# Kernel tuning notes

Measured on AMD Instinct MI355X. Metric: run time of the kernel, lower is better.

## Reference

```python
import jax, jax.numpy as jnp
import numpy as np

D_MODEL = 1024
N_TILES = 16
BATCH = 32768
THRESH = 0.3


def setup_inputs() -> dict:
    key = jax.random.key(0)
    k_x, k_sig, k_w, k_b = jax.random.split(key, 4)
    x = jax.random.normal(k_x, (BATCH, D_MODEL), dtype=jnp.float32)
    # nn.Parameter(torch.randn(n_tiles, d_model) * 0.5)
    signatures_raw = jax.random.normal(k_sig, (N_TILES, D_MODEL), dtype=jnp.float32) * 0.5
    # nn.Linear(d_model, d_model) default init: U(-1/sqrt(fan_in), 1/sqrt(fan_in))
    bound = 1.0 / np.sqrt(D_MODEL)
    W = jax.random.uniform(k_w, (N_TILES, D_MODEL, D_MODEL), dtype=jnp.float32, minval=-bound, maxval=bound)
    b = jax.random.uniform(k_b, (N_TILES, D_MODEL), dtype=jnp.float32, minval=-bound, maxval=bound)
    return {"x": x, "signatures_raw": signatures_raw, "W": W, "b": b}


def _quantize_ternary(s):
    # straight-through ternary: forward value is q, gradient is identity
    q = jnp.where(s > THRESH, 1.0, jnp.where(s < -THRESH, -1.0, 0.0))
    return s + jax.lax.stop_gradient(q - s)


def reference(x, signatures_raw, W, b):
    sigs = _quantize_ternary(signatures_raw)          # [E, D]
    scores = x @ sigs.T                               # [B, E]
    tile_indices = jnp.argmax(scores, axis=-1)        # [B]
    out = jnp.zeros_like(x)
    # fixed small loop over experts: masked combine of per-expert Linear+ReLU
    for e in range(N_TILES):
        y = jax.nn.relu(x @ W[e].T + b[e])            # [B, D]
        out = out + jnp.where((tile_indices == e)[:, None], y, 0.0)
    out = out + x                                     # residual
    return out, tile_indices
```

## Files before the change

kernel.cpp:

```cpp
#include <hip/hip_runtime.h>
#include <hip/hip_bf16.h>

#define BATCH   32768
#define DM      1024
#define NE      16
#define THRESHF 0.3f
#define MARGIN  0.02f

#define CTRL_OFF 131072
#define QBF_OFF  139264
#define PERM_OFF 172032
#define XBF_OFF  311296
#define WB_OFF   67420160ull
#define WS_NEED  (WB_OFF + (size_t)NE * DM * DM * 2)

typedef __attribute__((ext_vector_type(8))) short bf16x8;
typedef __attribute__((ext_vector_type(4))) float f32x4;

static __device__ __forceinline__ unsigned short f2bf(float f) {
    union { float f; unsigned u; } v; v.f = f;
    unsigned r = (v.u + 0x7FFFu + ((v.u >> 16) & 1u)) >> 16;
    return (unsigned short)r;
}
static __device__ __forceinline__ float bf2f(unsigned short h) {
    union { unsigned u; float f; } v; v.u = ((unsigned)h) << 16;
    return v.f;
}

static __device__ __forceinline__ void gload_lds16(const void* g, void* s) {
    __builtin_amdgcn_global_load_lds(
        (const __attribute__((address_space(1))) void*)g,
        (__attribute__((address_space(3))) void*)s, 16, 0, 0);
}

__global__ void k_init(const float* __restrict__ sig, unsigned* __restrict__ ctrl,
                       int* __restrict__ perm, unsigned short* __restrict__ Qbf) {
    const int t = blockIdx.x * 256 + threadIdx.x;
    if (t < 544) ctrl[t] = 0;
    if (t < 1024) {
        unsigned pm = 0, mm = 0;
#pragma unroll
        for (int e = 0; e < NE; ++e) {
            float s = sig[e * DM + t];
            pm |= (s > THRESHF ? 1u : 0u) << e;
            mm |= (s < -THRESHF ? 1u : 0u) << e;
        }
        ctrl[1024 + t] = pm | (mm << 16);
    }
    if (t < 8704) ((int4*)perm)[t] = make_int4(0, 0, 0, 0);
    {
        float s = sig[t];
        Qbf[t] = s > THRESHF ? (unsigned short)0x3F80u
                             : (s < -THRESHF ? (unsigned short)0xBF80u : (unsigned short)0u);
    }
}

__global__ __launch_bounds__(256) void k_router(const float* __restrict__ x,
                                                const unsigned short* __restrict__ Qbf,
                                                unsigned* __restrict__ ctrl,
                                                int* __restrict__ idx,
                                                float* __restrict__ outIdx,
                                                unsigned short* __restrict__ Xbf,
                                                int writeXbf) {
    const int t = threadIdx.x, w = t >> 6, l = t & 63;
    const int lc = l & 15, lr = l >> 4;
    const int wid = blockIdx.x * 4 + w;
    const int row0 = wid * 16;
    const unsigned* packT = ctrl + 1024;

    const float* ax = x + (size_t)(row0 + lc) * DM + lr * 8;
    const unsigned short* qx = Qbf + (size_t)lc * DM + lr * 8;
    unsigned short* xb = Xbf + (size_t)(row0 + lc) * DM + lr * 8;

    f32x4 acc = (f32x4){0.f, 0.f, 0.f, 0.f};

    for (int kt = 0; kt < 16; ++kt) {
#pragma unroll
        for (int h = 0; h < 2; ++h) {
            const int ko = kt * 64 + h * 32;
            float4 v0 = *(const float4*)(ax + ko);
            float4 v1 = *(const float4*)(ax + ko + 4);
            bf16x8 q = *(const bf16x8*)(qx + ko);

            float f[8] = {v0.x, v0.y, v0.z, v0.w, v1.x, v1.y, v1.z, v1.w};
            bf16x8 ah, al;
#pragma unroll
            for (int j = 0; j < 8; ++j) {
                unsigned short hi = f2bf(f[j]);
                float r = f[j] - bf2f(hi);
                ah[j] = (short)hi;
                al[j] = (short)f2bf(r);
            }
            if (writeXbf) *(bf16x8*)(xb + ko) = ah;
            acc = __builtin_amdgcn_mfma_f32_16x16x32_bf16(ah, q, acc, 0, 0, 0);
            acc = __builtin_amdgcn_mfma_f32_16x16x32_bf16(al, q, acc, 0, 0, 0);
        }
    }

    float bv[4]; int bi[4]; float gap[4];
#pragma unroll
    for (int reg = 0; reg < 4; ++reg) {
        float v = acc[reg]; int i = lc; float s = -3.4e38f;
#pragma unroll
        for (int m = 1; m < 16; m <<= 1) {
            float ov = __shfl_xor(v, m, 64);
            int oi = __shfl_xor(i, m, 64);
            float os = __shfl_xor(s, m, 64);
            bool take = (ov > v) || (ov == v && oi < i);
            float loser = take ? v : ov;
            v = take ? ov : v;
            i = take ? oi : i;
            s = fmaxf(fmaxf(s, os), loser);
        }
        bv[reg] = v; bi[reg] = i; gap[reg] = v - s;
    }

    unsigned flagsw = 0;
#pragma unroll
    for (int reg = 0; reg < 4; ++reg)
        flagsw |= (gap[reg] < MARGIN ? 1u : 0u) << reg;

    if (__any(lc == 0 && flagsw != 0)) {
#pragma unroll
        for (int reg = 0; reg < 4; ++reg) {
            for (int g = 0; g < 4; ++g) {
                const unsigned fw = __shfl(flagsw, g * 16, 64);
                if ((fw >> reg) & 1u) {
                    const int row = row0 + g * 4 + reg;
                    const float* xr = x + (size_t)row * DM;
                    float xv[16]; unsigned mk[16];
#pragma unroll
                    for (int k2 = 0; k2 < 16; ++k2) {
                        xv[k2] = xr[k2 * 64 + l];
                        mk[k2] = packT[k2 * 64 + l];
                    }
                    double best = 0.0; int bbi = 0;
                    for (int e = 0; e < 16; ++e) {
                        double a = 0.0;
#pragma unroll
                        for (int k2 = 0; k2 < 16; ++k2) {
                            const int pb = (int)((mk[k2] >> e) & 1u);
                            const int mb = (int)((mk[k2] >> (16 + e)) & 1u);
                            a += pb ? (double)xv[k2] : (mb ? -(double)xv[k2] : 0.0);
                        }
#pragma unroll
                        for (int m = 1; m < 64; m <<= 1) a += __shfl_xor(a, m, 64);
                        if (e == 0 || a > best) { best = a; bbi = e; }
                    }
                    if (lr == g && lc == 0) bi[reg] = bbi;
                }
            }
        }
    }

    if (lc == 0) {
#pragma unroll
        for (int reg = 0; reg < 4; ++reg) {
            const int row = row0 + lr * 4 + reg;
            idx[row] = bi[reg];
            outIdx[row] = (float)bi[reg];
            atomicAdd(&ctrl[bi[reg] * 16], 1u);
        }
    }
}

__global__ void k_scan(unsigned* __restrict__ ctrl) {
    if (threadIdx.x == 0) {
        int* tileBase = (int*)(ctrl + 512);
        int acc = 0;
        for (int e = 0; e < NE; ++e) {
            tileBase[e] = acc;
            acc += (int)((ctrl[e * 16] + 127u) / 128u);
        }
        tileBase[NE] = acc;
    }
}

__global__ __launch_bounds__(256) void k_perm(const int* __restrict__ idx,
                                              unsigned* __restrict__ ctrl,
                                              int* __restrict__ perm) {
    __shared__ unsigned hcnt[16];
    __shared__ unsigned hbase[16];
    const int t = threadIdx.x;
    const int row = blockIdx.x * 256 + t;
    const int* tileBase = (const int*)(ctrl + 512);
    if (t < 16) hcnt[t] = 0;
    __syncthreads();
    const int e = idx[row];
    const unsigned lrank = atomicAdd(&hcnt[e], 1u);
    __syncthreads();
    if (t < 16) hbase[t] = atomicAdd(&ctrl[256 + t * 16], hcnt[t]);
    __syncthreads();
    perm[tileBase[e] * 128 + hbase[e] + lrank] = row;
}

__global__ __launch_bounds__(256) void k_convw(const float* __restrict__ W,
                                               unsigned short* __restrict__ Wb) {
    const size_t g = ((size_t)blockIdx.x * 256 + threadIdx.x) * 8;
    float4 a = *(const float4*)&W[g];
    float4 b = *(const float4*)&W[g + 4];
    *(ushort4*)&Wb[g]     = make_ushort4(f2bf(a.x), f2bf(a.y), f2bf(a.z), f2bf(a.w));
    *(ushort4*)&Wb[g + 4] = make_ushort4(f2bf(b.x), f2bf(b.y), f2bf(b.z), f2bf(b.w));
}

template <int MODE>
__global__ __launch_bounds__(256) void k_gemm(const unsigned short* __restrict__ Xbf,
                                              const unsigned short* __restrict__ Wb,
                                              const float* __restrict__ x,
                                              const float* __restrict__ W,
                                              const float* __restrict__ bias,
                                              const int* __restrict__ perm,
                                              const unsigned* __restrict__ ctrl,
                                              float* __restrict__ out) {
    __shared__ unsigned short A_lds[3][128 * 32];
    __shared__ unsigned short B_lds[3][128 * 32];

    const int* tileBase = (const int*)(ctrl + 512);

    int bx, ny;
    {
        const int flat = blockIdx.x;
        const int xcd = flat & 7, s2 = flat >> 3;
        bx = xcd * 34 + (s2 >> 3);
        ny = s2 & 7;
    }
    const int total = tileBase[NE];
    if (bx >= total) return;
    int e = 0;
    while (e < NE - 1 && tileBase[e + 1] <= bx) ++e;
    const int ltile = bx - tileBase[e];
    const int valid = (int)ctrl[e * 16] - ltile * 128;
    const int n0 = ny * 128;

    const int t = threadIdx.x, w = t >> 6, l = t & 63;
    const int wr = w >> 1, wc = w & 1;
    const int lc = l & 15, lr = l >> 4;
    const int hsw = ((t & 3) - ((t >> 3) & 3)) & 3;
    const int ssw = (lr + (lc >> 1)) & 3;

    f32x4 acc[4][4];
#pragma unroll
    for (int m = 0; m < 4; ++m)
#pragma unroll
        for (int n = 0; n < 4; ++n) acc[m][n] = (f32x4){0.f, 0.f, 0.f, 0.f};

    const size_t aRowBase = (size_t)bx * 128;
    const unsigned short* Bg = Wb + ((size_t)e * DM + n0) * DM;

    if (MODE == 0) {
        const int r0 = t >> 2;
        const int prow0 = perm[aRowBase + r0];
        const int prow1 = perm[aRowBase + 64 + r0];
        const unsigned short* a0 = Xbf + (size_t)prow0 * DM + hsw * 8;
        const unsigned short* a1 = Xbf + (size_t)prow1 * DM + hsw * 8;
        const unsigned short* b0 = Bg + (size_t)(t >> 2) * DM + hsw * 8;
        const unsigned short* b1 = Bg + (size_t)(64 + (t >> 2)) * DM + hsw * 8;

        auto STAGE = [&](int kt, int buf) {
            const int ko = kt * 32;
            gload_lds16(a0 + ko, &A_lds[buf][(size_t)(w * 64) * 8]);
            gload_lds16(a1 + ko, &A_lds[buf][(size_t)(256 + w * 64) * 8]);
            gload_lds16(b0 + ko, &B_lds[buf][(size_t)(w * 64) * 8]);
            gload_lds16(b1 + ko, &B_lds[buf][(size_t)(256 + w * 64) * 8]);
        };

        STAGE(0, 0);
        STAGE(1, 1);

        const int NT = DM / 32;
        int cur = 0;
        for (int kt = 0; kt < NT; ++kt) {
            if (kt + 1 < NT) asm volatile("s_waitcnt vmcnt(4)" ::: "memory");
            else             asm volatile("s_waitcnt vmcnt(0)" ::: "memory");
            __builtin_amdgcn_sched_barrier(0);
            __builtin_amdgcn_s_barrier();
            __builtin_amdgcn_sched_barrier(0);

            if (kt + 2 < NT) {
                const int nb = (cur + 2 >= 3) ? cur - 1 : cur + 2;
                STAGE(kt + 2, nb);
            }

            bf16x8 af[4], bf[4];
#pragma unroll
            for (int m = 0; m < 4; ++m)
                af[m] = *(const bf16x8*)&A_lds[cur][(wr * 64 + m * 16 + lc) * 32 + ssw * 8];
#pragma unroll
            for (int n = 0; n < 4; ++n)
                bf[n] = *(const bf16x8*)&B_lds[cur][(wc * 64 + n * 16 + lc) * 32 + ssw * 8];
#pragma unroll
            for (int m = 0; m < 4; ++m)
#pragma unroll
                for (int n = 0; n < 4; ++n)
                    acc[m][n] = __builtin_amdgcn_mfma_f32_16x16x32_bf16(af[m], bf[n], acc[m][n], 0, 0, 0);

            cur = (cur + 1 >= 3) ? 0 : cur + 1;
        }
    } else {
        for (int kt = 0; kt < DM / 32; ++kt) {
            __syncthreads();
#pragma unroll
            for (int rd = 0; rd < 2; ++rd) {
                const int c = rd * 256 + t;
                const int r = c >> 2;
                const float* wp = W + ((size_t)e * DM + n0 + r) * DM + kt * 32 + hsw * 8;
                float4 q0 = *(const float4*)wp;
                float4 q1 = *(const float4*)(wp + 4);
                *(ushort4*)&B_lds[0][c * 8]     = make_ushort4(f2bf(q0.x), f2bf(q0.y), f2bf(q0.z), f2bf(q0.w));
                *(ushort4*)&B_lds[0][c * 8 + 4] = make_ushort4(f2bf(q1.x), f2bf(q1.y), f2bf(q1.z), f2bf(q1.w));
                ushort4 p0 = make_ushort4(0, 0, 0, 0), p1 = p0;
                if (r < valid) {
                    const int orow = perm[aRowBase + r];
                    const float* xp = x + (size_t)orow * DM + kt * 32 + hsw * 8;
                    float4 u0 = *(const float4*)xp;
                    float4 u1 = *(const float4*)(xp + 4);
                    p0 = make_ushort4(f2bf(u0.x), f2bf(u0.y), f2bf(u0.z), f2bf(u0.w));
                    p1 = make_ushort4(f2bf(u1.x), f2bf(u1.y), f2bf(u1.z), f2bf(u1.w));
                }
                *(ushort4*)&A_lds[0][c * 8]     = p0;
                *(ushort4*)&A_lds[0][c * 8 + 4] = p1;
            }
            __syncthreads();

            bf16x8 af[4], bf[4];
#pragma unroll
            for (int m = 0; m < 4; ++m)
                af[m] = *(const bf16x8*)&A_lds[0][(wr * 64 + m * 16 + lc) * 32 + ssw * 8];
#pragma unroll
            for (int n = 0; n < 4; ++n)
                bf[n] = *(const bf16x8*)&B_lds[0][(wc * 64 + n * 16 + lc) * 32 + ssw * 8];
#pragma unroll
            for (int m = 0; m < 4; ++m)
#pragma unroll
                for (int n = 0; n < 4; ++n)
                    acc[m][n] = __builtin_amdgcn_mfma_f32_16x16x32_bf16(af[m], bf[n], acc[m][n], 0, 0, 0);
        }
    }

    float bvv[4];
#pragma unroll
    for (int n = 0; n < 4; ++n) bvv[n] = bias[e * DM + n0 + wc * 64 + n * 16 + lc];

#pragma unroll
    for (int m = 0; m < 4; ++m) {
#pragma unroll
        for (int reg = 0; reg < 4; ++reg) {
            const int rit = wr * 64 + m * 16 + lr * 4 + reg;
            if (rit < valid) {
                const int orow = perm[aRowBase + rit];
                float* op = out + (size_t)orow * DM;
                if (MODE == 0) {
                    const unsigned short* xr = Xbf + (size_t)orow * DM;
#pragma unroll
                    for (int n = 0; n < 4; ++n) {
                        const int col = n0 + wc * 64 + n * 16 + lc;
                        float v = acc[m][n][reg] + bvv[n];
                        v = v > 0.f ? v : 0.f;
                        op[col] = v + bf2f(xr[col]);
                    }
                } else {
                    const float* xr = x + (size_t)orow * DM;
#pragma unroll
                    for (int n = 0; n < 4; ++n) {
                        const int col = n0 + wc * 64 + n * 16 + lc;
                        float v = acc[m][n][reg] + bvv[n];
                        v = v > 0.f ? v : 0.f;
                        op[col] = v + xr[col];
                    }
                }
            }
        }
    }
}

extern "C" void kernel_launch(void* const* d_in, const int* in_sizes, int n_in,
                              void* d_out, int out_size, void* d_ws, size_t ws_size,
                              hipStream_t stream) {
    const float* x    = (const float*)d_in[0];
    const float* sig  = (const float*)d_in[1];
    const float* W    = (const float*)d_in[2];
    const float* bias = (const float*)d_in[3];
    float* out = (float*)d_out;
    float* outIdx = out + (size_t)BATCH * DM;

    char* ws = (char*)d_ws;
    int* idx = (int*)ws;
    unsigned* ctrl = (unsigned*)(ws + CTRL_OFF);
    unsigned short* Qbf = (unsigned short*)(ws + QBF_OFF);
    int* perm = (int*)(ws + PERM_OFF);
    unsigned short* Xbf = (unsigned short*)(ws + XBF_OFF);
    unsigned short* Wb = (unsigned short*)(ws + WB_OFF);

    const bool full = ws_size >= WS_NEED;

    k_init<<<64, 256, 0, stream>>>(sig, ctrl, perm, Qbf);
    k_router<<<512, 256, 0, stream>>>(x, Qbf, ctrl, idx, outIdx, Xbf, full ? 1 : 0);
    k_scan<<<1, 64, 0, stream>>>(ctrl);
    k_perm<<<128, 256, 0, stream>>>(idx, ctrl, perm);
    if (full) {
        k_convw<<<8192, 256, 0, stream>>>(W, Wb);
        k_gemm<0><<<2176, 256, 0, stream>>>(Xbf, Wb, x, W, bias, perm, ctrl, out);
    } else {
        k_gemm<1><<<2176, 256, 0, stream>>>(Xbf, Wb, x, W, bias, perm, ctrl, out);
    }
}
```

Before: 247.8 us.

## Replace 128x128 expert GEMM with 256x256 tile, 512-thread double-buffered kernel

Replaces the grouped expert GEMM with a new kernel using 256x256 output tiles, 8 waves, a double-buffered LDS pipeline with a K-step of 64, swizzled LDS addressing, interleaved async global-to-LDS loads, and setprio around MFMA bursts. Routing groups are padded to 256 rows, so perm and scan take a group size G. The larger tiles are meant to raise arithmetic intensity and cut L2/HBM traffic for A and B. The cost is more padding waste per expert, fewer blocks (576), and higher register and LDS pressure.

```diff
diff --git a/kernel.cpp b/kernel.cpp
--- a/kernel.cpp
+++ b/kernel.cpp
@@ -10,12 +10,14 @@
 #define CTRL_OFF 131072
 #define QBF_OFF  139264
 #define PERM_OFF 172032
-#define XBF_OFF  311296
-#define WB_OFF   67420160ull
+#define XBF_OFF  319488
+#define WB_OFF   67428352ull
 #define WS_NEED  (WB_OFF + (size_t)NE * DM * DM * 2)
 
 typedef __attribute__((ext_vector_type(8))) short bf16x8;
 typedef __attribute__((ext_vector_type(4))) float f32x4;
+
+#define MFMA16(a, b, c) __builtin_amdgcn_mfma_f32_16x16x32_bf16(a, b, c, 0, 0, 0)
 
 static __device__ __forceinline__ unsigned short f2bf(float f) {
     union { float f; unsigned u; } v; v.f = f;
@@ -47,7 +49,7 @@
         }
         ctrl[1024 + t] = pm | (mm << 16);
     }
-    if (t < 8704) ((int4*)perm)[t] = make_int4(0, 0, 0, 0);
+    if (t < 9216) ((int4*)perm)[t] = make_int4(0, 0, 0, 0);
     {
         float s = sig[t];
         Qbf[t] = s > THRESHF ? (unsigned short)0x3F80u
@@ -92,8 +94,8 @@
                 al[j] = (short)f2bf(r);
             }
             if (writeXbf) *(bf16x8*)(xb + ko) = ah;
-            acc = __builtin_amdgcn_mfma_f32_16x16x32_bf16(ah, q, acc, 0, 0, 0);
-            acc = __builtin_amdgcn_mfma_f32_16x16x32_bf16(al, q, acc, 0, 0, 0);
+            acc = MFMA16(ah, q, acc);
+            acc = MFMA16(al, q, acc);
         }
     }
 
@@ -164,13 +166,13 @@
     }
 }
 
-__global__ void k_scan(unsigned* __restrict__ ctrl) {
+__global__ void k_scan(unsigned* __restrict__ ctrl, int G) {
     if (threadIdx.x == 0) {
         int* tileBase = (int*)(ctrl + 512);
         int acc = 0;
         for (int e = 0; e < NE; ++e) {
             tileBase[e] = acc;
-            acc += (int)((ctrl[e * 16] + 127u) / 128u);
+            acc += (int)((ctrl[e * 16] + (unsigned)(G - 1)) / (unsigned)G);
         }
         tileBase[NE] = acc;
     }
@@ -178,7 +180,7 @@
 
 __global__ __launch_bounds__(256) void k_perm(const int* __restrict__ idx,
                                               unsigned* __restrict__ ctrl,
-                                              int* __restrict__ perm) {
+                                              int* __restrict__ perm, int G) {
     __shared__ unsigned hcnt[16];
     __shared__ unsigned hbase[16];
     const int t = threadIdx.x;
@@ -191,7 +193,7 @@
     __syncthreads();
     if (t < 16) hbase[t] = atomicAdd(&ctrl[256 + t * 16], hcnt[t]);
     __syncthreads();
-    perm[tileBase[e] * 128 + hbase[e] + lrank] = row;
+    perm[tileBase[e] * G + hbase[e] + lrank] = row;
 }
 
 __global__ __launch_bounds__(256) void k_convw(const float* __restrict__ W,
@@ -203,20 +205,208 @@
     *(ushort4*)&Wb[g + 4] = make_ushort4(f2bf(b.x), f2bf(b.y), f2bf(b.z), f2bf(b.w));
 }
 
-template <int MODE>
-__global__ __launch_bounds__(256) void k_gemm(const unsigned short* __restrict__ Xbf,
-                                              const unsigned short* __restrict__ Wb,
-                                              const float* __restrict__ x,
-                                              const float* __restrict__ W,
-                                              const float* __restrict__ bias,
-                                              const int* __restrict__ perm,
-                                              const unsigned* __restrict__ ctrl,
-                                              float* __restrict__ out) {
-    __shared__ unsigned short A_lds[3][128 * 32];
-    __shared__ unsigned short B_lds[3][128 * 32];
+#define LDA(Ab, mf, ks) \
+    (*(const bf16x8*)&(Ab)[(((wr * 128 + (mf) * 16 + lc) * 8 + \
+                             (((ks) * 4 + lr + (lc & 7)) & 7)) * 8)])
+#define LDB(Bb, nf, ks) \
+    (*(const bf16x8*)&(Bb)[(((wc * 64 + (nf) * 16 + lc) * 8 + \
+                             (((ks) * 4 + lr + (lc & 7)) & 7)) * 8)])
+
+__global__ __launch_bounds__(512, 2) void k_gemm256(
+        const unsigned short* __restrict__ Xbf,
+        const unsigned short* __restrict__ Wb,
+        const float* __restrict__ bias,
+        const int* __restrict__ perm,
+        const unsigned* __restrict__ ctrl,
+        float* __restrict__ out) {
+    __shared__ unsigned short Al[2][16384];
+    __shared__ unsigned short Bl[2][16384];
 
     const int* tileBase = (const int*)(ctrl + 512);
-
+    int bx, ny;
+    {
+        const int flat = blockIdx.x;
+        const int xcd = flat & 7, s2 = flat >> 3;
+        bx = xcd * 18 + (s2 >> 2);
+        ny = s2 & 3;
+    }
+    const int total = tileBase[NE];
+    if (bx >= total) return;
+    int e = 0;
+    while (e < NE - 1 && tileBase[e + 1] <= bx) ++e;
+    const int valid = (int)ctrl[e * 16] - (bx - tileBase[e]) * 256;
+    const int n0 = ny * 256;
+
+    const int t = threadIdx.x, w = t >> 6, l = t & 63;
+    const int lc = l & 15, lr = l >> 4;
+    const int wr = w >> 2, wc = w & 3;
+    const int j = (w << 3) + (l >> 3);
+    const int d = ((l & 7) - (l >> 3)) & 7;
+    const size_t prB = (size_t)bx * 256;
+
+    const unsigned short* asrc[4];
+    const unsigned short* bsrc[4];
+    int aB[4], bB[4];
+#pragma unroll
+    for (int q = 0; q < 4; ++q) {
+        const int ra = q * 32 + (j & 31) + (j >> 5) * 128;
+        asrc[q] = Xbf + (size_t)perm[prB + ra] * DM + d * 8;
+        const int rb = (j >> 4) * 64 + q * 16 + (j & 15);
+        bsrc[q] = Wb + ((size_t)e * DM + n0 + rb) * DM + d * 8;
+        aB[q] = (q * 256 + (w >> 2) * 1024 + (w & 3) * 64) * 8;
+        bB[q] = ((w >> 1) * 512 + q * 128 + (w & 1) * 64) * 8;
+    }
+
+    f32x4 acc[8][4];
+#pragma unroll
+    for (int m = 0; m < 8; ++m)
+#pragma unroll
+        for (int n = 0; n < 4; ++n) acc[m][n] = (f32x4){0.f, 0.f, 0.f, 0.f};
+
+#pragma unroll
+    for (int q = 0; q < 4; ++q) gload_lds16(bsrc[q], &Bl[0][bB[q]]);
+#pragma unroll
+    for (int q = 0; q < 4; ++q) gload_lds16(asrc[q], &Al[0][aB[q]]);
+
+    const int NT = DM / 64;
+    for (int kt = 0; kt < NT; ++kt) {
+        const int buf = kt & 1;
+        const unsigned short* Ab = Al[buf];
+        const unsigned short* Bb = Bl[buf];
+        unsigned short* An = Al[buf ^ 1];
+        unsigned short* Bn = Bl[buf ^ 1];
+        const int ko = (kt + 1) * 64;
+        const bool more = (kt + 1 < NT);
+
+        if (more) {
+            gload_lds16(bsrc[0] + ko, Bn + bB[0]);
+            gload_lds16(bsrc[1] + ko, Bn + bB[1]);
+            asm volatile("s_waitcnt vmcnt(2)" ::: "memory");
+        } else {
+            asm volatile("s_waitcnt vmcnt(0)" ::: "memory");
+        }
+        __builtin_amdgcn_sched_barrier(0);
+        __builtin_amdgcn_s_barrier();
+        __builtin_amdgcn_sched_barrier(0);
+
+        bf16x8 bfr[4][2];
+#pragma unroll
+        for (int nf = 0; nf < 4; ++nf) {
+            bfr[nf][0] = LDB(Bb, nf, 0);
+            bfr[nf][1] = LDB(Bb, nf, 1);
+        }
+        {
+            bf16x8 a00 = LDA(Ab, 0, 0), a01 = LDA(Ab, 0, 1);
+            bf16x8 a10 = LDA(Ab, 1, 0), a11 = LDA(Ab, 1, 1);
+            __builtin_amdgcn_s_setprio(1);
+#pragma unroll
+            for (int nf = 0; nf < 4; ++nf) {
+                acc[0][nf] = MFMA16(a00, bfr[nf][0], acc[0][nf]);
+                acc[0][nf] = MFMA16(a01, bfr[nf][1], acc[0][nf]);
+                acc[1][nf] = MFMA16(a10, bfr[nf][0], acc[1][nf]);
+                acc[1][nf] = MFMA16(a11, bfr[nf][1], acc[1][nf]);
+            }
+            __builtin_amdgcn_s_setprio(0);
+        }
+        __builtin_amdgcn_s_barrier();
+
+        {
+            bf16x8 a00 = LDA(Ab, 2, 0), a01 = LDA(Ab, 2, 1);
+            bf16x8 a10 = LDA(Ab, 3, 0), a11 = LDA(Ab, 3, 1);
+            if (more) {
+                gload_lds16(bsrc[2] + ko, Bn + bB[2]);
+                gload_lds16(bsrc[3] + ko, Bn + bB[3]);
+            }
+            __builtin_amdgcn_s_barrier();
+            __builtin_amdgcn_sched_barrier(0);
+            __builtin_amdgcn_s_setprio(1);
+#pragma unroll
+            for (int nf = 0; nf < 4; ++nf) {
+                acc[2][nf] = MFMA16(a00, bfr[nf][0], acc[2][nf]);
+                acc[2][nf] = MFMA16(a01, bfr[nf][1], acc[2][nf]);
+                acc[3][nf] = MFMA16(a10, bfr[nf][0], acc[3][nf]);
+                acc[3][nf] = MFMA16(a11, bfr[nf][1], acc[3][nf]);
+            }
+            __builtin_amdgcn_s_setprio(0);
+        }
+        __builtin_amdgcn_s_barrier();
+
+        {
+            bf16x8 a00 = LDA(Ab, 4, 0), a01 = LDA(Ab, 4, 1);
+            bf16x8 a10 = LDA(Ab, 5, 0), a11 = LDA(Ab, 5, 1);
+            if (more) {
+                gload_lds16(asrc[0] + ko, An + aB[0]);
+                gload_lds16(asrc[1] + ko, An + aB[1]);
+            }
+            __builtin_amdgcn_s_barrier();
+            __builtin_amdgcn_sched_barrier(0);
+            __builtin_amdgcn_s_setprio(1);
+#pragma unroll
+            for (int nf = 0; nf < 4; ++nf) {
+                acc[4][nf] = MFMA16(a00, bfr[nf][0], acc[4][nf]);
+                acc[4][nf] = MFMA16(a01, bfr[nf][1], acc[4][nf]);
+                acc[5][nf] = MFMA16(a10, bfr[nf][0], acc[5][nf]);
+                acc[5][nf] = MFMA16(a11, bfr[nf][1], acc[5][nf]);
+            }
+            __builtin_amdgcn_s_setprio(0);
+        }
+        __builtin_amdgcn_s_barrier();
+
+        {
+            bf16x8 a00 = LDA(Ab, 6, 0), a01 = LDA(Ab, 6, 1);
+            bf16x8 a10 = LDA(Ab, 7, 0), a11 = LDA(Ab, 7, 1);
+            if (more) {
+                gload_lds16(asrc[2] + ko, An + aB[2]);
+                gload_lds16(asrc[3] + ko, An + aB[3]);
+            }
+            __builtin_amdgcn_s_barrier();
+            __builtin_amdgcn_sched_barrier(0);
+            __builtin_amdgcn_s_setprio(1);
+#pragma unroll
+            for (int nf = 0; nf < 4; ++nf) {
+                acc[6][nf] = MFMA16(a00, bfr[nf][0], acc[6][nf]);
+                acc[6][nf] = MFMA16(a01, bfr[nf][1], acc[6][nf]);
+                acc[7][nf] = MFMA16(a10, bfr[nf][0], acc[7][nf]);
+                acc[7][nf] = MFMA16(a11, bfr[nf][1], acc[7][nf]);
+            }
+            __builtin_amdgcn_s_setprio(0);
+        }
+        __builtin_amdgcn_s_barrier();
+    }
+
+    float bvv[4];
+#pragma unroll
+    for (int nf = 0; nf < 4; ++nf)
+        bvv[nf] = bias[e * DM + n0 + wc * 64 + nf * 16 + lc];
+
+#pragma unroll
+    for (int mf = 0; mf < 8; ++mf) {
+#pragma unroll
+        for (int reg = 0; reg < 4; ++reg) {
+            const int rit = wr * 128 + mf * 16 + lr * 4 + reg;
+            if (rit < valid) {
+                const int orow = perm[prB + rit];
+                float* op = out + (size_t)orow * DM;
+                const unsigned short* xr = Xbf + (size_t)orow * DM;
+#pragma unroll
+                for (int nf = 0; nf < 4; ++nf) {
+                    const int col = n0 + wc * 64 + nf * 16 + lc;
+                    float v = acc[mf][nf][reg] + bvv[nf];
+                    v = v > 0.f ? v : 0.f;
+                    op[col] = v + bf2f(xr[col]);
+                }
+            }
+        }
+    }
+}
+
+__global__ __launch_bounds__(256) void k_gemm_small(
+        const float* __restrict__ x, const float* __restrict__ W,
+        const float* __restrict__ bias, const int* __restrict__ perm,
+        const unsigned* __restrict__ ctrl, float* __restrict__ out) {
+    __shared__ unsigned short A_lds[128 * 32];
+    __shared__ unsigned short B_lds[128 * 32];
+    const int* tileBase = (const int*)(ctrl + 512);
     int bx, ny;
     {
         const int flat = blockIdx.x;
@@ -228,10 +418,8 @@
     if (bx >= total) return;
     int e = 0;
     while (e < NE - 1 && tileBase[e + 1] <= bx) ++e;
-    const int ltile = bx - tileBase[e];
-    const int valid = (int)ctrl[e * 16] - ltile * 128;
+    const int valid = (int)ctrl[e * 16] - (bx - tileBase[e]) * 128;
     const int n0 = ny * 128;
-
     const int t = threadIdx.x, w = t >> 6, l = t & 63;
     const int wr = w >> 1, wc = w & 1;
     const int lc = l & 15, lr = l >> 4;
@@ -243,134 +431,67 @@
     for (int m = 0; m < 4; ++m)
 #pragma unroll
         for (int n = 0; n < 4; ++n) acc[m][n] = (f32x4){0.f, 0.f, 0.f, 0.f};
-
     const size_t aRowBase = (size_t)bx * 128;
-    const unsigned short* Bg = Wb + ((size_t)e * DM + n0) * DM;
-
-    if (MODE == 0) {
-        const int r0 = t >> 2;
-        const int prow0 = perm[aRowBase + r0];
-        const int prow1 = perm[aRowBase + 64 + r0];
-        const unsigned short* a0 = Xbf + (size_t)prow0 * DM + hsw * 8;
-        const unsigned short* a1 = Xbf + (size_t)prow1 * DM + hsw * 8;
-        const unsigned short* b0 = Bg + (size_t)(t >> 2) * DM + hsw * 8;
-        const unsigned short* b1 = Bg + (size_t)(64 + (t >> 2)) * DM + hsw * 8;
-
-        auto STAGE = [&](int kt, int buf) {
-            const int ko = kt * 32;
-            gload_lds16(a0 + ko, &A_lds[buf][(size_t)(w * 64) * 8]);
-            gload_lds16(a1 + ko, &A_lds[buf][(size_t)(256 + w * 64) * 8]);
-            gload_lds16(b0 + ko, &B_lds[buf][(size_t)(w * 64) * 8]);
-            gload_lds16(b1 + ko, &B_lds[buf][(size_t)(256 + w * 64) * 8]);
-        };
-
-        STAGE(0, 0);
-        STAGE(1, 1);
-
-        const int NT = DM / 32;
-        int cur = 0;
-        for (int kt = 0; kt < NT; ++kt) {
-            if (kt + 1 < NT) asm volatile("s_waitcnt vmcnt(4)" ::: "memory");
-            else             asm volatile("s_waitcnt vmcnt(0)" ::: "memory");
-            __builtin_amdgcn_sched_barrier(0);
-            __builtin_amdgcn_s_barrier();
-            __builtin_amdgcn_sched_barrier(0);
-
-            if (kt + 2 < NT) {
-                const int nb = (cur + 2 >= 3) ? cur - 1 : cur + 2;
-                STAGE(kt + 2, nb);
-            }
-
-            bf16x8 af[4], bf[4];
-#pragma unroll
-            for (int m = 0; m < 4; ++m)
-                af[m] = *(const bf16x8*)&A_lds[cur][(wr * 64 + m * 16 + lc) * 32 + ssw * 8];
+
+    for (int kt = 0; kt < DM / 32; ++kt) {
+        __syncthreads();
+#pragma unroll
+        for (int rd = 0; rd < 2; ++rd) {
+            const int c = rd * 256 + t;
+            const int r = c >> 2;
+            const float* wp = W + ((size_t)e * DM + n0 + r) * DM + kt * 32 + hsw * 8;
+            float4 q0 = *(const float4*)wp;
+            float4 q1 = *(const float4*)(wp + 4);
+            *(ushort4*)&B_lds[c * 8]     = make_ushort4(f2bf(q0.x), f2bf(q0.y), f2bf(q0.z), f2bf(q0.w));
+            *(ushort4*)&B_lds[c * 8 + 4] = make_ushort4(f2bf(q1.x), f2bf(q1.y), f2bf(q1.z), f2bf(q1.w));
+            ushort4 p0 = make_ushort4(0, 0, 0, 0), p1 = p0;
+            if (r < valid) {
+                const int orow = perm[aRowBase + r];
+                const float* xp = x + (size_t)orow * DM + kt * 32 + hsw * 8;
+                float4 u0 = *(const float4*)xp;
+                float4 u1 = *(const float4*)(xp + 4);
+                p0 = make_ushort4(f2bf(u0.x), f2bf(u0.y), f2bf(u0.z), f2bf(u0.w));
+                p1 = make_ushort4(f2bf(u1.x), f2bf(u1.y), f2bf(u1.z), f2bf(u1.w));
+            }
+            *(ushort4*)&A_lds[c * 8]     = p0;
+            *(ushort4*)&A_lds[c * 8 + 4] = p1;
+        }
+        __syncthreads();
+        bf16x8 af[4], bf[4];
+#pragma unroll
+        for (int m = 0; m < 4; ++m)
+            af[m] = *(const bf16x8*)&A_lds[(wr * 64 + m * 16 + lc) * 32 + ssw * 8];
+#pragma unroll
+        for (int n = 0; n < 4; ++n)
+            bf[n] = *(const bf16x8*)&B_lds[(wc * 64 + n * 16 + lc) * 32 + ssw * 8];
+#pragma unroll
+        for (int m = 0; m < 4; ++m)
 #pragma unroll
             for (int n = 0; n < 4; ++n)
-                bf[n] = *(const bf16x8*)&B_lds[cur][(wc * 64 + n * 16 + lc) * 32 + ssw * 8];
-#pragma unroll
-            for (int m = 0; m < 4; ++m)
-#pragma unroll
-                for (int n = 0; n < 4; ++n)
-                    acc[m][n] = __builtin_amdgcn_mfma_f32_16x16x32_bf16(af[m], bf[n], acc[m][n], 0, 0, 0);
-
-            cur = (cur + 1 >= 3) ? 0 : cur + 1;
-        }
-    } else {
-        for (int kt = 0; kt < DM / 32; ++kt) {
-            __syncthreads();
-#pragma unroll
-            for (int rd = 0; rd < 2; ++rd) {
-                const int c = rd * 256 + t;
-                const int r = c >> 2;
-                const float* wp = W + ((size_t)e * DM + n0 + r) * DM + kt * 32 + hsw * 8;
-                float4 q0 = *(const float4*)wp;
-                float4 q1 = *(const float4*)(wp + 4);
-                *(ushort4*)&B_lds[0][c * 8]     = make_ushort4(f2bf(q0.x), f2bf(q0.y), f2bf(q0.z), f2bf(q0.w));
-                *(ushort4*)&B_lds[0][c * 8 + 4] = make_ushort4(f2bf(q1.x), f2bf(q1.y), f2bf(q1.z), f2bf(q1.w));
-                ushort4 p0 = make_ushort4(0, 0, 0, 0), p1 = p0;
-                if (r < valid) {
-                    const int orow = perm[aRowBase + r];
-                    const float* xp = x + (size_t)orow * DM + kt * 32 + hsw * 8;
-                    float4 u0 = *(const float4*)xp;
-                    float4 u1 = *(const float4*)(xp + 4);
-                    p0 = make_ushort4(f2bf(u0.x), f2bf(u0.y), f2bf(u0.z), f2bf(u0.w));
-                    p1 = make_ushort4(f2bf(u1.x), f2bf(u1.y), f2bf(u1.z), f2bf(u1.w));
-                }
-                *(ushort4*)&A_lds[0][c * 8]     = p0;
-                *(ushort4*)&A_lds[0][c * 8 + 4] = p1;
-            }
-            __syncthreads();
-
-            bf16x8 af[4], bf[4];
-#pragma unroll
-            for (int m = 0; m < 4; ++m)
-                af[m] = *(const bf16x8*)&A_lds[0][(wr * 64 + m * 16 + lc) * 32 + ssw * 8];
-#pragma unroll
-            for (int n = 0; n < 4; ++n)
-                bf[n] = *(const bf16x8*)&B_lds[0][(wc * 64 + n * 16 + lc) * 32 + ssw * 8];
-#pragma unroll
-            for (int m = 0; m < 4; ++m)
-#pragma unroll
-                for (int n = 0; n < 4; ++n)
-                    acc[m][n] = __builtin_amdgcn_mfma_f32_16x16x32_bf16(af[m], bf[n], acc[m][n], 0, 0, 0);
-        }
+                acc[m][n] = MFMA16(af[m], bf[n], acc[m][n]);
     }
 
     float bvv[4];
 #pragma unroll
     for (int n = 0; n < 4; ++n) bvv[n] = bias[e * DM + n0 + wc * 64 + n * 16 + lc];
-
-#pragma unroll
-    for (int m = 0; m < 4; ++m) {
+#pragma unroll
+    for (int m = 0; m < 4; ++m)
 #pragma unroll
         for (int reg = 0; reg < 4; ++reg) {
             const int rit = wr * 64 + m * 16 + lr * 4 + reg;
             if (rit < valid) {
                 const int orow = perm[aRowBase + rit];
+                const float* xr = x + (size_t)orow * DM;
                 float* op = out + (size_t)orow * DM;
-                if (MODE == 0) {
-                    const unsigned short* xr = Xbf + (size_t)orow * DM;
-#pragma unroll
-                    for (int n = 0; n < 4; ++n) {
-                        const int col = n0 + wc * 64 + n * 16 + lc;
-                        float v = acc[m][n][reg] + bvv[n];
-                        v = v > 0.f ? v : 0.f;
-                        op[col] = v + bf2f(xr[col]);
-                    }
-                } else {
-                    const float* xr = x + (size_t)orow * DM;
-#pragma unroll
-                    for (int n = 0; n < 4; ++n) {
-                        const int col = n0 + wc * 64 + n * 16 + lc;
-                        float v = acc[m][n][reg] + bvv[n];
-                        v = v > 0.f ? v : 0.f;
-                        op[col] = v + xr[col];
-                    }
+#pragma unroll
+                for (int n = 0; n < 4; ++n) {
+                    const int col = n0 + wc * 64 + n * 16 + lc;
+                    float v = acc[m][n][reg] + bvv[n];
+                    v = v > 0.f ? v : 0.f;
+                    op[col] = v + xr[col];
                 }
             }
         }
-    }
 }
 
 extern "C" void kernel_launch(void* const* d_in, const int* in_sizes, int n_in,
@@ -392,15 +513,16 @@
     unsigned short* Wb = (unsigned short*)(ws + WB_OFF);
 
     const bool full = ws_size >= WS_NEED;
+    const int G = full ? 256 : 128;
 
     k_init<<<64, 256, 0, stream>>>(sig, ctrl, perm, Qbf);
     k_router<<<512, 256, 0, stream>>>(x, Qbf, ctrl, idx, outIdx, Xbf, full ? 1 : 0);
-    k_scan<<<1, 64, 0, stream>>>(ctrl);
-    k_perm<<<128, 256, 0, stream>>>(idx, ctrl, perm);
+    k_scan<<<1, 64, 0, stream>>>(ctrl, G);
+    k_perm<<<128, 256, 0, stream>>>(idx, ctrl, perm, G);
     if (full) {
         k_convw<<<8192, 256, 0, stream>>>(W, Wb);
-        k_gemm<0><<<2176, 256, 0, stream>>>(Xbf, Wb, x, W, bias, perm, ctrl, out);
+        k_gemm256<<<576, 512, 0, stream>>>(Xbf, Wb, bias, perm, ctrl, out);
     } else {
-        k_gemm<1><<<2176, 256, 0, stream>>>(Xbf, Wb, x, W, bias, perm, ctrl, out);
-    }
-}
+        k_gemm_small<<<2176, 256, 0, stream>>>(x, W, bias, perm, ctrl, out);
+    }
+}
```

Result: slower. 280.1 us (+13.1%).

## Fuse scan/perm/weight-convert kernels and shrink GEMM B-buffering for occupancy

Applied to the files above, without the earlier changes.

Removes the single-thread scan kernel by having each block recompute tile bases from the expert counts, and merges the permutation kernel with the fp32-to-bf16 weight conversion into one launch. The main GEMM drops to double-buffered B tiles (A stays triple-buffered) with a reworked prefetch schedule and a launch bound of 4 blocks per CU to reduce LDS use and raise occupancy. Launch overhead and serialization between small kernels should drop, at the cost of redundant tile-base computation per block and a shallower B prefetch.

```diff
diff --git a/kernel.cpp b/kernel.cpp
--- a/kernel.cpp
+++ b/kernel.cpp
@@ -10,12 +10,14 @@
 #define CTRL_OFF 131072
 #define QBF_OFF  139264
 #define PERM_OFF 172032
-#define XBF_OFF  311296
-#define WB_OFF   67420160ull
+#define XBF_OFF  319488
+#define WB_OFF   67428352ull
 #define WS_NEED  (WB_OFF + (size_t)NE * DM * DM * 2)
 
 typedef __attribute__((ext_vector_type(8))) short bf16x8;
 typedef __attribute__((ext_vector_type(4))) float f32x4;
+
+#define MFMA16(a, b, c) __builtin_amdgcn_mfma_f32_16x16x32_bf16(a, b, c, 0, 0, 0)
 
 static __device__ __forceinline__ unsigned short f2bf(float f) {
     union { float f; unsigned u; } v; v.f = f;
@@ -31,6 +33,17 @@
     __builtin_amdgcn_global_load_lds(
         (const __attribute__((address_space(1))) void*)g,
         (__attribute__((address_space(3))) void*)s, 16, 0, 0);
+}
+
+static __device__ __forceinline__ int tile_base(const unsigned* ctrl, int* tb) {
+    int acc = 0;
+#pragma unroll
+    for (int e = 0; e < NE; ++e) {
+        tb[e] = acc;
+        acc += (int)((ctrl[e * 16] + 127u) >> 7);
+    }
+    tb[NE] = acc;
+    return acc;
 }
 
 __global__ void k_init(const float* __restrict__ sig, unsigned* __restrict__ ctrl,
@@ -47,7 +60,7 @@
         }
         ctrl[1024 + t] = pm | (mm << 16);
     }
-    if (t < 8704) ((int4*)perm)[t] = make_int4(0, 0, 0, 0);
+    if (t < 9216) ((int4*)perm)[t] = make_int4(0, 0, 0, 0);
     {
         float s = sig[t];
         Qbf[t] = s > THRESHF ? (unsigned short)0x3F80u
@@ -92,8 +105,8 @@
                 al[j] = (short)f2bf(r);
             }
             if (writeXbf) *(bf16x8*)(xb + ko) = ah;
-            acc = __builtin_amdgcn_mfma_f32_16x16x32_bf16(ah, q, acc, 0, 0, 0);
-            acc = __builtin_amdgcn_mfma_f32_16x16x32_bf16(al, q, acc, 0, 0, 0);
+            acc = MFMA16(ah, q, acc);
+            acc = MFMA16(al, q, acc);
         }
     }
 
@@ -164,26 +177,25 @@
     }
 }
 
-__global__ void k_scan(unsigned* __restrict__ ctrl) {
-    if (threadIdx.x == 0) {
-        int* tileBase = (int*)(ctrl + 512);
-        int acc = 0;
-        for (int e = 0; e < NE; ++e) {
-            tileBase[e] = acc;
-            acc += (int)((ctrl[e * 16] + 127u) / 128u);
-        }
-        tileBase[NE] = acc;
-    }
-}
-
-__global__ __launch_bounds__(256) void k_perm(const int* __restrict__ idx,
-                                              unsigned* __restrict__ ctrl,
-                                              int* __restrict__ perm) {
+__global__ __launch_bounds__(256) void k_permconv(const int* __restrict__ idx,
+                                                  unsigned* __restrict__ ctrl,
+                                                  int* __restrict__ perm,
+                                                  const float* __restrict__ W,
+                                                  unsigned short* __restrict__ Wb) {
+    if (blockIdx.x >= 128) {
+        const size_t g = ((size_t)(blockIdx.x - 128) * 256 + threadIdx.x) * 8;
+        float4 a = *(const float4*)&W[g];
+        float4 b = *(const float4*)&W[g + 4];
+        *(ushort4*)&Wb[g]     = make_ushort4(f2bf(a.x), f2bf(a.y), f2bf(a.z), f2bf(a.w));
+        *(ushort4*)&Wb[g + 4] = make_ushort4(f2bf(b.x), f2bf(b.y), f2bf(b.z), f2bf(b.w));
+        return;
+    }
     __shared__ unsigned hcnt[16];
     __shared__ unsigned hbase[16];
     const int t = threadIdx.x;
     const int row = blockIdx.x * 256 + t;
-    const int* tileBase = (const int*)(ctrl + 512);
+    int tb[NE + 1];
+    tile_base(ctrl, tb);
     if (t < 16) hcnt[t] = 0;
     __syncthreads();
     const int e = idx[row];
@@ -191,31 +203,21 @@
     __syncthreads();
     if (t < 16) hbase[t] = atomicAdd(&ctrl[256 + t * 16], hcnt[t]);
     __syncthreads();
-    perm[tileBase[e] * 128 + hbase[e] + lrank] = row;
-}
-
-__global__ __launch_bounds__(256) void k_convw(const float* __restrict__ W,
-                                               unsigned short* __restrict__ Wb) {
-    const size_t g = ((size_t)blockIdx.x * 256 + threadIdx.x) * 8;
-    float4 a = *(const float4*)&W[g];
-    float4 b = *(const float4*)&W[g + 4];
-    *(ushort4*)&Wb[g]     = make_ushort4(f2bf(a.x), f2bf(a.y), f2bf(a.z), f2bf(a.w));
-    *(ushort4*)&Wb[g + 4] = make_ushort4(f2bf(b.x), f2bf(b.y), f2bf(b.z), f2bf(b.w));
-}
-
-template <int MODE>
-__global__ __launch_bounds__(256) void k_gemm(const unsigned short* __restrict__ Xbf,
-                                              const unsigned short* __restrict__ Wb,
-                                              const float* __restrict__ x,
-                                              const float* __restrict__ W,
-                                              const float* __restrict__ bias,
-                                              const int* __restrict__ perm,
-                                              const unsigned* __restrict__ ctrl,
-                                              float* __restrict__ out) {
+    perm[tb[e] * 128 + hbase[e] + lrank] = row;
+}
+
+__global__ __launch_bounds__(256, 4) void k_gemm(
+        const unsigned short* __restrict__ Xbf,
+        const unsigned short* __restrict__ Wb,
+        const float* __restrict__ bias,
+        const int* __restrict__ perm,
+        const unsigned* __restrict__ ctrl,
+        float* __restrict__ out) {
     __shared__ unsigned short A_lds[3][128 * 32];
-    __shared__ unsigned short B_lds[3][128 * 32];
-
-    const int* tileBase = (const int*)(ctrl + 512);
+    __shared__ unsigned short B_lds[2][128 * 32];
+
+    int tb[NE + 1];
+    const int total = tile_base(ctrl, tb);
 
     int bx, ny;
     {
@@ -224,12 +226,10 @@
         bx = xcd * 34 + (s2 >> 3);
         ny = s2 & 7;
     }
-    const int total = tileBase[NE];
     if (bx >= total) return;
     int e = 0;
-    while (e < NE - 1 && tileBase[e + 1] <= bx) ++e;
-    const int ltile = bx - tileBase[e];
-    const int valid = (int)ctrl[e * 16] - ltile * 128;
+    while (e < NE - 1 && tb[e + 1] <= bx) ++e;
+    const int valid = (int)ctrl[e * 16] - (bx - tb[e]) * 128;
     const int n0 = ny * 128;
 
     const int t = threadIdx.x, w = t >> 6, l = t & 63;
@@ -247,94 +247,53 @@
     const size_t aRowBase = (size_t)bx * 128;
     const unsigned short* Bg = Wb + ((size_t)e * DM + n0) * DM;
 
-    if (MODE == 0) {
-        const int r0 = t >> 2;
-        const int prow0 = perm[aRowBase + r0];
-        const int prow1 = perm[aRowBase + 64 + r0];
-        const unsigned short* a0 = Xbf + (size_t)prow0 * DM + hsw * 8;
-        const unsigned short* a1 = Xbf + (size_t)prow1 * DM + hsw * 8;
-        const unsigned short* b0 = Bg + (size_t)(t >> 2) * DM + hsw * 8;
-        const unsigned short* b1 = Bg + (size_t)(64 + (t >> 2)) * DM + hsw * 8;
-
-        auto STAGE = [&](int kt, int buf) {
-            const int ko = kt * 32;
-            gload_lds16(a0 + ko, &A_lds[buf][(size_t)(w * 64) * 8]);
-            gload_lds16(a1 + ko, &A_lds[buf][(size_t)(256 + w * 64) * 8]);
-            gload_lds16(b0 + ko, &B_lds[buf][(size_t)(w * 64) * 8]);
-            gload_lds16(b1 + ko, &B_lds[buf][(size_t)(256 + w * 64) * 8]);
-        };
-
-        STAGE(0, 0);
-        STAGE(1, 1);
-
-        const int NT = DM / 32;
-        int cur = 0;
-        for (int kt = 0; kt < NT; ++kt) {
-            if (kt + 1 < NT) asm volatile("s_waitcnt vmcnt(4)" ::: "memory");
-            else             asm volatile("s_waitcnt vmcnt(0)" ::: "memory");
-            __builtin_amdgcn_sched_barrier(0);
-            __builtin_amdgcn_s_barrier();
-            __builtin_amdgcn_sched_barrier(0);
-
-            if (kt + 2 < NT) {
-                const int nb = (cur + 2 >= 3) ? cur - 1 : cur + 2;
-                STAGE(kt + 2, nb);
-            }
-
-            bf16x8 af[4], bf[4];
-#pragma unroll
-            for (int m = 0; m < 4; ++m)
-                af[m] = *(const bf16x8*)&A_lds[cur][(wr * 64 + m * 16 + lc) * 32 + ssw * 8];
+    const int r0 = t >> 2;
+    const int prow0 = perm[aRowBase + r0];
+    const int prow1 = perm[aRowBase + 64 + r0];
+    const unsigned short* a0 = Xbf + (size_t)prow0 * DM + hsw * 8;
+    const unsigned short* a1 = Xbf + (size_t)prow1 * DM + hsw * 8;
+    const unsigned short* b0 = Bg + (size_t)(t >> 2) * DM + hsw * 8;
+    const unsigned short* b1 = Bg + (size_t)(64 + (t >> 2)) * DM + hsw * 8;
+
+    auto STAGE_A = [&](int kt, int buf) {
+        const int ko = kt * 32;
+        gload_lds16(a0 + ko, &A_lds[buf][(size_t)(w * 64) * 8]);
+        gload_lds16(a1 + ko, &A_lds[buf][(size_t)(256 + w * 64) * 8]);
+    };
+    auto STAGE_B = [&](int kt, int buf) {
+        const int ko = kt * 32;
+        gload_lds16(b0 + ko, &B_lds[buf][(size_t)(w * 64) * 8]);
+        gload_lds16(b1 + ko, &B_lds[buf][(size_t)(256 + w * 64) * 8]);
+    };
+
+    STAGE_A(0, 0);
+    STAGE_B(0, 0);
+    STAGE_A(1, 1);
+
+    const int NT = DM / 32;
+    for (int kt = 0; kt < NT; ++kt) {
+        if (kt + 1 < NT) asm volatile("s_waitcnt vmcnt(2)" ::: "memory");
+        else             asm volatile("s_waitcnt vmcnt(0)" ::: "memory");
+        __builtin_amdgcn_sched_barrier(0);
+        __builtin_amdgcn_s_barrier();
+        __builtin_amdgcn_sched_barrier(0);
+
+        const int ba = kt % 3, bb = kt & 1;
+        if (kt + 1 < NT) STAGE_B(kt + 1, bb ^ 1);
+        if (kt + 2 < NT) STAGE_A(kt + 2, (ba + 2 >= 3) ? ba - 1 : ba + 2);
+
+        bf16x8 af[4], bf[4];
+#pragma unroll
+        for (int m = 0; m < 4; ++m)
+            af[m] = *(const bf16x8*)&A_lds[ba][(wr * 64 + m * 16 + lc) * 32 + ssw * 8];
+#pragma unroll
+        for (int n = 0; n < 4; ++n)
+            bf[n] = *(const bf16x8*)&B_lds[bb][(wc * 64 + n * 16 + lc) * 32 + ssw * 8];
+#pragma unroll
+        for (int m = 0; m < 4; ++m)
 #pragma unroll
             for (int n = 0; n < 4; ++n)
-                bf[n] = *(const bf16x8*)&B_lds[cur][(wc * 64 + n * 16 + lc) * 32 + ssw * 8];
-#pragma unroll
-            for (int m = 0; m < 4; ++m)
-#pragma unroll
-                for (int n = 0; n < 4; ++n)
-                    acc[m][n] = __builtin_amdgcn_mfma_f32_16x16x32_bf16(af[m], bf[n], acc[m][n], 0, 0, 0);
-
-            cur = (cur + 1 >= 3) ? 0 : cur + 1;
-        }
-    } else {
-        for (int kt = 0; kt < DM / 32; ++kt) {
-            __syncthreads();
-#pragma unroll
-            for (int rd = 0; rd < 2; ++rd) {
-                const int c = rd * 256 + t;
-                const int r = c >> 2;
-                const float* wp = W + ((size_t)e * DM + n0 + r) * DM + kt * 32 + hsw * 8;
-                float4 q0 = *(const float4*)wp;
-                float4 q1 = *(const float4*)(wp + 4);
-                *(ushort4*)&B_lds[0][c * 8]     = make_ushort4(f2bf(q0.x), f2bf(q0.y), f2bf(q0.z), f2bf(q0.w));
-                *(ushort4*)&B_lds[0][c * 8 + 4] = make_ushort4(f2bf(q1.x), f2bf(q1.y), f2bf(q1.z), f2bf(q1.w));
-                ushort4 p0 = make_ushort4(0, 0, 0, 0), p1 = p0;
-                if (r < valid) {
-                    const int orow = perm[aRowBase + r];
-                    const float* xp = x + (size_t)orow * DM + kt * 32 + hsw * 8;
-                    float4 u0 = *(const float4*)xp;
-                    float4 u1 = *(const float4*)(xp + 4);
-                    p0 = make_ushort4(f2bf(u0.x), f2bf(u0.y), f2bf(u0.z), f2bf(u0.w));
-                    p1 = make_ushort4(f2bf(u1.x), f2bf(u1.y), f2bf(u1.z), f2bf(u1.w));
-                }
-                *(ushort4*)&A_lds[0][c * 8]     = p0;
-                *(ushort4*)&A_lds[0][c * 8 + 4] = p1;
-            }
-            __syncthreads();
-
-            bf16x8 af[4], bf[4];
-#pragma unroll
-            for (int m = 0; m < 4; ++m)
-                af[m] = *(const bf16x8*)&A_lds[0][(wr * 64 + m * 16 + lc) * 32 + ssw * 8];
-#pragma unroll
-            for (int n = 0; n < 4; ++n)
-                bf[n] = *(const bf16x8*)&B_lds[0][(wc * 64 + n * 16 + lc) * 32 + ssw * 8];
-#pragma unroll
-            for (int m = 0; m < 4; ++m)
-#pragma unroll
-                for (int n = 0; n < 4; ++n)
-                    acc[m][n] = __builtin_amdgcn_mfma_f32_16x16x32_bf16(af[m], bf[n], acc[m][n], 0, 0, 0);
-        }
+                acc[m][n] = MFMA16(af[m], bf[n], acc[m][n]);
     }
 
     float bvv[4];
@@ -349,28 +308,111 @@
             if (rit < valid) {
                 const int orow = perm[aRowBase + rit];
                 float* op = out + (size_t)orow * DM;
-                if (MODE == 0) {
-                    const unsigned short* xr = Xbf + (size_t)orow * DM;
-#pragma unroll
-                    for (int n = 0; n < 4; ++n) {
-                        const int col = n0 + wc * 64 + n * 16 + lc;
-                        float v = acc[m][n][reg] + bvv[n];
-                        v = v > 0.f ? v : 0.f;
-                        op[col] = v + bf2f(xr[col]);
-                    }
-                } else {
-                    const float* xr = x + (size_t)orow * DM;
-#pragma unroll
-                    for (int n = 0; n < 4; ++n) {
-                        const int col = n0 + wc * 64 + n * 16 + lc;
-                        float v = acc[m][n][reg] + bvv[n];
-                        v = v > 0.f ? v : 0.f;
-                        op[col] = v + xr[col];
-                    }
+                const unsigned short* xr = Xbf + (size_t)orow * DM;
+#pragma unroll
+                for (int n = 0; n < 4; ++n) {
+                    const int col = n0 + wc * 64 + n * 16 + lc;
+                    float v = acc[m][n][reg] + bvv[n];
+                    v = v > 0.f ? v : 0.f;
+                    op[col] = v + bf2f(xr[col]);
                 }
             }
         }
     }
+}
+
+__global__ __launch_bounds__(256) void k_gemm_small(
+        const float* __restrict__ x, const float* __restrict__ W,
+        const float* __restrict__ bias, const int* __restrict__ perm,
+        const unsigned* __restrict__ ctrl, float* __restrict__ out) {
+    __shared__ unsigned short A_lds[128 * 32];
+    __shared__ unsigned short B_lds[128 * 32];
+    int tb[NE + 1];
+    const int total = tile_base(ctrl, tb);
+    int bx, ny;
+    {
+        const int flat = blockIdx.x;
+        const int xcd = flat & 7, s2 = flat >> 3;
+        bx = xcd * 34 + (s2 >> 3);
+        ny = s2 & 7;
+    }
+    if (bx >= total) return;
+    int e = 0;
+    while (e < NE - 1 && tb[e + 1] <= bx) ++e;
+    const int valid = (int)ctrl[e * 16] - (bx - tb[e]) * 128;
+    const int n0 = ny * 128;
+    const int t = threadIdx.x, w = t >> 6, l = t & 63;
+    const int wr = w >> 1, wc = w & 1;
+    const int lc = l & 15, lr = l >> 4;
+    const int hsw = ((t & 3) - ((t >> 3) & 3)) & 3;
+    const int ssw = (lr + (lc >> 1)) & 3;
+
+    f32x4 acc[4][4];
+#pragma unroll
+    for (int m = 0; m < 4; ++m)
+#pragma unroll
+        for (int n = 0; n < 4; ++n) acc[m][n] = (f32x4){0.f, 0.f, 0.f, 0.f};
+    const size_t aRowBase = (size_t)bx * 128;
+
+    for (int kt = 0; kt < DM / 32; ++kt) {
+        __syncthreads();
+#pragma unroll
+        for (int rd = 0; rd < 2; ++rd) {
+            const int c = rd * 256 + t;
+            const int r = c >> 2;
+            const float* wp = W + ((size_t)e * DM + n0 + r) * DM + kt * 32 + hsw * 8;
+            float4 q0 = *(const float4*)wp;
+            float4 q1 = *(const float4*)(wp + 4);
+            *(ushort4*)&B_lds[c * 8]     = make_ushort4(f2bf(q0.x), f2bf(q0.y), f2bf(q0.z), f2bf(q0.w));
+            *(ushort4*)&B_lds[c * 8 + 4] = make_ushort4(f2bf(q1.x), f2bf(q1.y), f2bf(q1.z), f2bf(q1.w));
+            ushort4 p0 = make_ushort4(0, 0, 0, 0), p1 = p0;
+            if (r < valid) {
+                const int orow = perm[aRowBase + r];
+                const float* xp = x + (size_t)orow * DM + kt * 32 + hsw * 8;
+                float4 u0 = *(const float4*)xp;
+                float4 u1 = *(const float4*)(xp + 4);
+                p0 = make_ushort4(f2bf(u0.x), f2bf(u0.y), f2bf(u0.z), f2bf(u0.w));
+                p1 = make_ushort4(f2bf(u1.x), f2bf(u1.y), f2bf(u1.z), f2bf(u1.w));
+            }
+            *(ushort4*)&A_lds[c * 8]     = p0;
+            *(ushort4*)&A_lds[c * 8 + 4] = p1;
+        }
+        __syncthreads();
+        bf16x8 af[4], bf[4];
+#pragma unroll
+        for (int m = 0; m < 4; ++m)
+            af[m] = *(const bf16x8*)&A_lds[(wr * 64 + m * 16 + lc) * 32 + ssw * 8];
+#pragma unroll
+        for (int n = 0; n < 4; ++n)
+            bf[n] = *(const bf16x8*)&B_lds[(wc * 64 + n * 16 + lc) * 32 + ssw * 8];
+#pragma unroll
+        for (int m = 0; m < 4; ++m)
+#pragma unroll
+            for (int n = 0; n < 4; ++n)
+                acc[m][n] = MFMA16(af[m], bf[n], acc[m][n]);
+    }
+
+    float bvv[4];
+#pragma unroll
+    for (int n = 0; n < 4; ++n) bvv[n] = bias[e * DM + n0 + wc * 64 + n * 16 + lc];
+#pragma unroll
+    for (int m = 0; m < 4; ++m)
+#pragma unroll
+        for (int reg = 0; reg < 4; ++reg) {
+            const int rit = wr * 64 + m * 16 + lr * 4 + reg;
+            if (rit < valid) {
+                const int orow = perm[aRowBase + rit];
+                const float* xr = x + (size_t)orow * DM;
+                float* op = out + (size_t)orow * DM;
+#pragma unroll
+                for (int n = 0; n < 4; ++n) {
+                    const int col = n0 + wc * 64 + n * 16 + lc;
+                    float v = acc[m][n][reg] + bvv[n];
+                    v = v > 0.f ? v : 0.f;
+                    op[col] = v + xr[col];
+                }
+            }
+        }
 }
 
 extern "C" void kernel_launch(void* const* d_in, const int* in_sizes, int n_in,
@@ -395,12 +437,10 @@
 
     k_init<<<64, 256, 0, stream>>>(sig, ctrl, perm, Qbf);
     k_router<<<512, 256, 0, stream>>>(x, Qbf, ctrl, idx, outIdx, Xbf, full ? 1 : 0);
-    k_scan<<<1, 64, 0, stream>>>(ctrl);
-    k_perm<<<128, 256, 0, stream>>>(idx, ctrl, perm);
+    k_permconv<<<full ? 8320 : 128, 256, 0, stream>>>(idx, ctrl, perm, W, Wb);
     if (full) {
-        k_convw<<<8192, 256, 0, stream>>>(W, Wb);
-        k_gemm<0><<<2176, 256, 0, stream>>>(Xbf, Wb, x, W, bias, perm, ctrl, out);
+        k_gemm<<<2176, 256, 0, stream>>>(Xbf, Wb, bias, perm, ctrl, out);
     } else {
-        k_gemm<1><<<2176, 256, 0, stream>>>(Xbf, Wb, x, W, bias, perm, ctrl, out);
-    }
-}
+        k_gemm_small<<<2176, 256, 0, stream>>>(x, W, bias, perm, ctrl, out);
+    }
+}
```

Result: slower. 255.3 us (+3.0%).
